# Kernel tuning notes

Measured on AMD Instinct MI355X. Metric: run time of the kernel, lower is better.

Reference implementation:

```python
import jax, jax.numpy as jnp
import numpy as np

NEG_INF = -1e9
LRELU_SLOPE = 0.2


def setup_inputs() -> dict:
    N, F_IN, F_OUT = 8192, 256, 128
    key = jax.random.key(0)
    k_adj, k_x, k_w, k_phi = jax.random.split(key, 4)
    adj = (jax.random.uniform(k_adj, (N, N)) < 0.01).astype(jnp.float32)
    x = jax.random.normal(k_x, (N, F_IN), dtype=jnp.float32)
    stdv_w = 1.0 / np.sqrt(F_OUT)
    weight = jax.random.uniform(k_w, (F_IN, F_OUT), minval=-stdv_w, maxval=stdv_w, dtype=jnp.float32)
    bias = jnp.zeros((F_OUT,), dtype=jnp.float32)
    phi = jax.random.uniform(k_phi, (2 * F_OUT, 1), minval=-1.0, maxval=1.0, dtype=jnp.float32)
    return {"adj": adj, "input": x, "weight": weight, "bias": bias, "phi": phi}


def reference(adj, input, weight, bias, phi):
    # x_prime: [N, F_OUT]
    x_prime = input @ weight + bias
    N = adj.shape[0]
    F_out = x_prime.shape[1]
    # S[i, j] = cat(x_i, x_j) @ phi = x_i @ phi[:F] + x_j @ phi[F:]
    # (identical math to the repeat+cat formulation, without the O(N^2*2F) tensor)
    phi_src = phi[:F_out, 0]  # [F_OUT]
    phi_dst = phi[F_out:, 0]  # [F_OUT]
    s_src = x_prime @ phi_src  # [N]
    s_dst = x_prime @ phi_dst  # [N]
    S = s_src[:, None] + s_dst[None, :]  # [N, N]
    S = jnp.where(S >= 0, S, LRELU_SLOPE * S)  # leaky_relu(0.2)
    mask = (adj + jnp.eye(N, dtype=adj.dtype)) > 0
    S_masked = jnp.where(mask, S, NEG_INF)
    attention = jax.nn.softmax(S_masked, axis=1)  # row-wise
    h = attention @ x_prime  # [N, F_OUT]
    return h
```

## Files before the change

kernel.cpp:

```cpp
#include <hip/hip_runtime.h>

#define Nn    8192
#define FIN   256
#define FOUTc 128
#define MAXN  512

typedef float f32x4 __attribute__((ext_vector_type(4)));

__global__ __launch_bounds__(256) void k_xp(const float* __restrict__ x,
                                            const float* __restrict__ w,
                                            const float* __restrict__ bias,
                                            const float* __restrict__ phi,
                                            float* __restrict__ xp,
                                            float* __restrict__ s_src,
                                            float* __restrict__ s_dst)
{
    const int wave = blockIdx.x * 4 + (threadIdx.x >> 6);
    const int lane = threadIdx.x & 63;
    const int row0 = wave * 8;

    const float2 bv = ((const float2*)bias)[lane];
    const float2 ps = ((const float2*)phi)[lane];
    const float2 pd = ((const float2*)(phi + FOUTc))[lane];

    const float* xr = x + (size_t)row0 * FIN;
    float2 acc[8];
#pragma unroll
    for (int r = 0; r < 8; r++) acc[r] = make_float2(0.f, 0.f);

#pragma unroll 4
    for (int k = 0; k < FIN; k++) {
        const float2 wv = ((const float2*)(w + (size_t)k * FOUTc))[lane];
#pragma unroll
        for (int r = 0; r < 8; r++) {
            const float xv = xr[r * FIN + k];
            acc[r].x = fmaf(xv, wv.x, acc[r].x);
            acc[r].y = fmaf(xv, wv.y, acc[r].y);
        }
    }

#pragma unroll
    for (int r = 0; r < 8; r++) {
        const float2 h = make_float2(acc[r].x + bv.x, acc[r].y + bv.y);
        ((float2*)(xp + (size_t)(row0 + r) * FOUTc))[lane] = h;
        float a = h.x * ps.x + h.y * ps.y;
        float b = h.x * pd.x + h.y * pd.y;
#pragma unroll
        for (int off = 32; off > 0; off >>= 1) {
            a += __shfl_down(a, off, 64);
            b += __shfl_down(b, off, 64);
        }
        if (lane == 0) { s_src[row0 + r] = a; s_dst[row0 + r] = b; }
    }
}

__global__ __launch_bounds__(256) void k_agg(const float* __restrict__ adj,
                                             const float* __restrict__ xp,
                                             const float* __restrict__ s_src,
                                             const float* __restrict__ s_dst,
                                             float* __restrict__ out)
{
    __shared__ int   nbr[MAXN];
    __shared__ float wts[MAXN];
    __shared__ float hp[2][FOUTc];
    __shared__ float sinv;
    __shared__ int   cnt;

    const int tid = threadIdx.x;
    const int i = blockIdx.x;
    if (tid == 0) cnt = 0;
    __syncthreads();

    const f32x4* arow4 = (const f32x4*)(adj + (size_t)i * Nn);
    f32x4 buf[8];
#pragma unroll
    for (int t = 0; t < 8; t++) buf[t] = __builtin_nontemporal_load(arow4 + t * 256 + tid);

#pragma unroll
    for (int t = 0; t < 8; t++) {
        const int j0 = (t * 256 + tid) * 4;
#pragma unroll
        for (int p = 0; p < 4; p++) {
            const int j = j0 + p;
            if (buf[t][p] != 0.f || j == i) {
                const int pos = atomicAdd(&cnt, 1);
                if (pos < MAXN) nbr[pos] = j;
            }
        }
    }
    __syncthreads();
    const int L    = (cnt < MAXN) ? cnt : MAXN;
    const int Lpad = (L + 7) & ~7;
    if (tid < Lpad - L) { nbr[L + tid] = i; wts[L + tid] = 0.f; }

    if (tid < 64) {
        const float ssi = s_src[i];
        float lmax = -1e30f;
        for (int n = tid; n < L; n += 64) {
            const float sd = s_dst[nbr[n]];
            wts[n] = sd;
            lmax = fmaxf(lmax, sd);
        }
#pragma unroll
        for (int off = 32; off > 0; off >>= 1)
            lmax = fmaxf(lmax, __shfl_xor(lmax, off, 64));
        const float Sm  = ssi + lmax;
        const float m_i = (Sm >= 0.f) ? Sm : 0.2f * Sm;
        float lsum = 0.f;
        for (int n = tid; n < L; n += 64) {
            float S = ssi + wts[n];
            S = (S >= 0.f) ? S : 0.2f * S;
            const float wv = __expf(S - m_i);
            wts[n] = wv;
            lsum += wv;
        }
#pragma unroll
        for (int off = 32; off > 0; off >>= 1) lsum += __shfl_xor(lsum, off, 64);
        if (tid == 0) sinv = 1.f / lsum;
    }
    __syncthreads();
    const float inv = sinv;

    const int o  = tid & 127;
    const int g  = tid >> 7;
    const int Lh = Lpad >> 1;
    const int base = g * Lh;
    const float* xpo = xp + o;
    float h0 = 0.f, h1 = 0.f, h2 = 0.f, h3 = 0.f;
    for (int n = base; n < base + Lh; n += 4) {
        const int   j0 = nbr[n],   j1 = nbr[n+1], j2 = nbr[n+2], j3 = nbr[n+3];
        const float w0 = wts[n],   w1 = wts[n+1], w2 = wts[n+2], w3 = wts[n+3];
        h0 = fmaf(w0, xpo[(size_t)j0 * FOUTc], h0);
        h1 = fmaf(w1, xpo[(size_t)j1 * FOUTc], h1);
        h2 = fmaf(w2, xpo[(size_t)j2 * FOUTc], h2);
        h3 = fmaf(w3, xpo[(size_t)j3 * FOUTc], h3);
    }
    hp[g][o] = (h0 + h1) + (h2 + h3);
    __syncthreads();
    if (tid < FOUTc)
        out[(size_t)i * FOUTc + tid] = (hp[0][tid] + hp[1][tid]) * inv;
}

extern "C" void kernel_launch(void* const* d_in, const int* in_sizes, int n_in,
                              void* d_out, int out_size, void* d_ws, size_t ws_size,
                              hipStream_t stream)
{
    (void)out_size; (void)ws_size;
    const float* adj  = (const float*)d_in[0];
    const float* x    = (const float*)d_in[1];
    const float* w    = (const float*)d_in[2];
    const float* bias = (const float*)d_in[3];
    const float* phi  = (const float*)d_in[4];
    for (int i = 0; i < n_in; i++) {
        switch (in_sizes[i]) {
            case Nn * Nn:     adj  = (const float*)d_in[i]; break;
            case Nn * FIN:    x    = (const float*)d_in[i]; break;
            case FIN * FOUTc: w    = (const float*)d_in[i]; break;
            case FOUTc:       bias = (const float*)d_in[i]; break;
            case 2 * FOUTc:   phi  = (const float*)d_in[i]; break;
        }
    }
    float* out = (float*)d_out;

    float* xp    = (float*)d_ws;
    float* s_src = xp + (size_t)Nn * FOUTc;
    float* s_dst = s_src + Nn;

    hipLaunchKernelGGL(k_xp,  dim3(256), dim3(256), 0, stream,
                       x, w, bias, phi, xp, s_src, s_dst);
    hipLaunchKernelGGL(k_agg, dim3(Nn),  dim3(256), 0, stream,
                       adj, xp, s_src, s_dst, out);
}
```

Baseline: 415.0 us.

## Warp-specialize aggregation: one wave compacts next adjacency row while others aggregate

The aggregation kernel now handles four rows per block with 192 threads. One wave scans and compacts the adjacency row for the next row into a double-buffered shared list, while two waves compute the softmax and the weighted gather for the current row. The goal is to overlap streaming the 256MB adjacency matrix with the gather and softmax work, and to cut per-block overhead. The tradeoff is that a single wave now streams each 32KB row, which may limit memory-level parallelism, and there are fewer blocks (2048) in flight.

Result: slower. 453.7 us (+9.3%).

```diff
diff --git a/kernel.cpp b/kernel.cpp
--- a/kernel.cpp
+++ b/kernel.cpp
@@ -4,6 +4,7 @@
 #define FIN   256
 #define FOUTc 128
 #define MAXN  512
+#define RPB   4
 
 typedef float f32x4 __attribute__((ext_vector_type(4)));
 
@@ -54,91 +55,123 @@
     }
 }
 
-__global__ __launch_bounds__(256) void k_agg(const float* __restrict__ adj,
+__device__ __forceinline__ void compact_row(const float* __restrict__ adj, int row,
+                                            int* __restrict__ nbrb, int* __restrict__ cnt,
+                                            int lane)
+{
+    const f32x4* arow4 = (const f32x4*)(adj + (size_t)row * Nn);
+#pragma unroll 1
+    for (int c = 0; c < 4; c++) {
+        f32x4 buf[8];
+#pragma unroll
+        for (int k = 0; k < 8; k++)
+            buf[k] = __builtin_nontemporal_load(arow4 + c * 512 + k * 64 + lane);
+#pragma unroll
+        for (int k = 0; k < 8; k++) {
+            const int j0 = (c * 512 + k * 64 + lane) * 4;
+#pragma unroll
+            for (int p = 0; p < 4; p++) {
+                const int j = j0 + p;
+                if (buf[k][p] != 0.f || j == row) {
+                    const int pos = atomicAdd(cnt, 1);
+                    if (pos < MAXN) nbrb[pos] = j;
+                }
+            }
+        }
+    }
+}
+
+__global__ __launch_bounds__(192) void k_agg(const float* __restrict__ adj,
                                              const float* __restrict__ xp,
                                              const float* __restrict__ s_src,
                                              const float* __restrict__ s_dst,
                                              float* __restrict__ out)
 {
-    __shared__ int   nbr[MAXN];
-    __shared__ float wts[MAXN];
-    __shared__ float hp[2][FOUTc];
-    __shared__ float sinv;
-    __shared__ int   cnt;
-
-    const int tid = threadIdx.x;
-    const int i = blockIdx.x;
-    if (tid == 0) cnt = 0;
+    __shared__ int   nbr[2][MAXN];
+    __shared__ float wts[2][MAXN];
+    __shared__ int   cnts[2];
+
+    const int tid  = threadIdx.x;
+    const int lane = tid & 63;
+    const int row0 = blockIdx.x * RPB;
+
+    if (tid == 0) { cnts[0] = 0; cnts[1] = 0; }
     __syncthreads();
 
-    const f32x4* arow4 = (const f32x4*)(adj + (size_t)i * Nn);
-    f32x4 buf[8];
-#pragma unroll
-    for (int t = 0; t < 8; t++) buf[t] = __builtin_nontemporal_load(arow4 + t * 256 + tid);
-
-#pragma unroll
-    for (int t = 0; t < 8; t++) {
-        const int j0 = (t * 256 + tid) * 4;
-#pragma unroll
-        for (int p = 0; p < 4; p++) {
-            const int j = j0 + p;
-            if (buf[t][p] != 0.f || j == i) {
-                const int pos = atomicAdd(&cnt, 1);
-                if (pos < MAXN) nbr[pos] = j;
-            }
-        }
-    }
+    if (tid >= 128) compact_row(adj, row0, nbr[0], &cnts[0], lane);
     __syncthreads();
-    const int L    = (cnt < MAXN) ? cnt : MAXN;
-    const int Lpad = (L + 7) & ~7;
-    if (tid < Lpad - L) { nbr[L + tid] = i; wts[L + tid] = 0.f; }
-
-    if (tid < 64) {
-        const float ssi = s_src[i];
-        float lmax = -1e30f;
-        for (int n = tid; n < L; n += 64) {
-            const float sd = s_dst[nbr[n]];
-            wts[n] = sd;
-            lmax = fmaxf(lmax, sd);
-        }
-#pragma unroll
-        for (int off = 32; off > 0; off >>= 1)
-            lmax = fmaxf(lmax, __shfl_xor(lmax, off, 64));
-        const float Sm  = ssi + lmax;
-        const float m_i = (Sm >= 0.f) ? Sm : 0.2f * Sm;
-        float lsum = 0.f;
-        for (int n = tid; n < L; n += 64) {
-            float S = ssi + wts[n];
-            S = (S >= 0.f) ? S : 0.2f * S;
-            const float wv = __expf(S - m_i);
-            wts[n] = wv;
-            lsum += wv;
-        }
-#pragma unroll
-        for (int off = 32; off > 0; off >>= 1) lsum += __shfl_xor(lsum, off, 64);
-        if (tid == 0) sinv = 1.f / lsum;
-    }
-    __syncthreads();
-    const float inv = sinv;
-
-    const int o  = tid & 127;
-    const int g  = tid >> 7;
-    const int Lh = Lpad >> 1;
-    const int base = g * Lh;
-    const float* xpo = xp + o;
-    float h0 = 0.f, h1 = 0.f, h2 = 0.f, h3 = 0.f;
-    for (int n = base; n < base + Lh; n += 4) {
-        const int   j0 = nbr[n],   j1 = nbr[n+1], j2 = nbr[n+2], j3 = nbr[n+3];
-        const float w0 = wts[n],   w1 = wts[n+1], w2 = wts[n+2], w3 = wts[n+3];
-        h0 = fmaf(w0, xpo[(size_t)j0 * FOUTc], h0);
-        h1 = fmaf(w1, xpo[(size_t)j1 * FOUTc], h1);
-        h2 = fmaf(w2, xpo[(size_t)j2 * FOUTc], h2);
-        h3 = fmaf(w3, xpo[(size_t)j3 * FOUTc], h3);
-    }
-    hp[g][o] = (h0 + h1) + (h2 + h3);
-    __syncthreads();
-    if (tid < FOUTc)
-        out[(size_t)i * FOUTc + tid] = (hp[0][tid] + hp[1][tid]) * inv;
+
+    for (int t = 0; t < RPB; t++) {
+        const int cur = t & 1;
+        const int row = row0 + t;
+
+        if (tid >= 128) {
+            if (t + 1 < RPB) {
+                const int nxt = cur ^ 1;
+                if (lane == 0) cnts[nxt] = 0;
+                compact_row(adj, row + 1, nbr[nxt], &cnts[nxt], lane);
+            }
+        } else {
+            const int Lr   = cnts[cur];
+            const int L    = (Lr < MAXN) ? Lr : MAXN;
+            const int Lpad = (L + 3) & ~3;
+            const float ssi = s_src[row];
+
+            float sdv[8];
+            float lmax = -1e30f;
+#pragma unroll
+            for (int q = 0; q < 8; q++) {
+                const int n = lane + 64 * q;
+                sdv[q] = -1e30f;
+                if (n < L) {
+                    sdv[q] = s_dst[nbr[cur][n]];
+                    lmax = fmaxf(lmax, sdv[q]);
+                }
+            }
+#pragma unroll
+            for (int off = 32; off > 0; off >>= 1)
+                lmax = fmaxf(lmax, __shfl_xor(lmax, off, 64));
+            const float Sm  = ssi + lmax;
+            const float m_i = (Sm >= 0.f) ? Sm : 0.2f * Sm;
+
+            float lsum = 0.f;
+#pragma unroll
+            for (int q = 0; q < 8; q++) {
+                const int n = lane + 64 * q;
+                if (n < L) {
+                    float S = ssi + sdv[q];
+                    S = (S >= 0.f) ? S : 0.2f * S;
+                    const float e = __expf(S - m_i);
+                    wts[cur][n] = e;
+                    lsum += e;
+                }
+            }
+#pragma unroll
+            for (int off = 32; off > 0; off >>= 1) lsum += __shfl_xor(lsum, off, 64);
+            const float inv = 1.f / lsum;
+
+            for (int n = L + lane; n < Lpad; n += 64) {
+                nbr[cur][n] = row;
+                wts[cur][n] = 0.f;
+            }
+
+            const int o = tid;
+            const float* xpo = xp + o;
+            float h0 = 0.f, h1 = 0.f, h2 = 0.f, h3 = 0.f;
+            for (int n = 0; n < Lpad; n += 4) {
+                const int   j0 = nbr[cur][n],     j1 = nbr[cur][n + 1];
+                const int   j2 = nbr[cur][n + 2], j3 = nbr[cur][n + 3];
+                const float w0 = wts[cur][n],     w1 = wts[cur][n + 1];
+                const float w2 = wts[cur][n + 2], w3 = wts[cur][n + 3];
+                h0 = fmaf(w0, xpo[(size_t)j0 * FOUTc], h0);
+                h1 = fmaf(w1, xpo[(size_t)j1 * FOUTc], h1);
+                h2 = fmaf(w2, xpo[(size_t)j2 * FOUTc], h2);
+                h3 = fmaf(w3, xpo[(size_t)j3 * FOUTc], h3);
+            }
+            out[(size_t)row * FOUTc + o] = ((h0 + h1) + (h2 + h3)) * inv;
+        }
+        __syncthreads();
+    }
 }
 
 extern "C" void kernel_launch(void* const* d_in, const int* in_sizes, int n_in,
@@ -166,8 +199,8 @@
     float* s_src = xp + (size_t)Nn * FOUTc;
     float* s_dst = s_src + Nn;
 
-    hipLaunchKernelGGL(k_xp,  dim3(256), dim3(256), 0, stream,
+    hipLaunchKernelGGL(k_xp,  dim3(256),    dim3(256), 0, stream,
                        x, w, bias, phi, xp, s_src, s_dst);
-    hipLaunchKernelGGL(k_agg, dim3(Nn),  dim3(256), 0, stream,
+    hipLaunchKernelGGL(k_agg, dim3(Nn/RPB), dim3(192), 0, stream,
                        adj, xp, s_src, s_dst, out);
 }
```

## Overlap adjacency compaction with feature projection and split aggregation into CSR pass

Applied to the files above, without the earlier changes.

The adjacency scan that builds per-row neighbor lists now runs inside the first kernel, alongside the x@W projection blocks. It writes a padded CSR-like list to workspace, so the dominant 256MB adjacency read can overlap with the GEMM instead of waiting for it. A second kernel reads the compact lists to do the softmax and aggregation, and the max/sum reductions now use all four waves instead of one. The cost is an extra round-trip of neighbor indices through global memory, an additional kernel, and more workspace use.

Result: no change. 412.9 us (-0.5%).

```diff
diff --git a/kernel.cpp b/kernel.cpp
--- a/kernel.cpp
+++ b/kernel.cpp
@@ -1,73 +1,71 @@
 #include <hip/hip_runtime.h>
 
-#define Nn    8192
-#define FIN   256
-#define FOUTc 128
-#define MAXN  512
+#define Nn     8192
+#define FIN    256
+#define FOUTc  128
+#define MAXN   512
+#define LCAP   504
+#define NXPB   256
 
 typedef float f32x4 __attribute__((ext_vector_type(4)));
 
-__global__ __launch_bounds__(256) void k_xp(const float* __restrict__ x,
-                                            const float* __restrict__ w,
-                                            const float* __restrict__ bias,
-                                            const float* __restrict__ phi,
-                                            float* __restrict__ xp,
-                                            float* __restrict__ s_src,
-                                            float* __restrict__ s_dst)
+__global__ __launch_bounds__(256) void k1(const float* __restrict__ adj,
+                                          const float* __restrict__ x,
+                                          const float* __restrict__ w,
+                                          const float* __restrict__ bias,
+                                          const float* __restrict__ phi,
+                                          float* __restrict__ xp,
+                                          float* __restrict__ s_src,
+                                          float* __restrict__ s_dst,
+                                          int* __restrict__ csr,
+                                          int* __restrict__ csr_cnt)
 {
-    const int wave = blockIdx.x * 4 + (threadIdx.x >> 6);
-    const int lane = threadIdx.x & 63;
-    const int row0 = wave * 8;
-
-    const float2 bv = ((const float2*)bias)[lane];
-    const float2 ps = ((const float2*)phi)[lane];
-    const float2 pd = ((const float2*)(phi + FOUTc))[lane];
-
-    const float* xr = x + (size_t)row0 * FIN;
-    float2 acc[8];
-#pragma unroll
-    for (int r = 0; r < 8; r++) acc[r] = make_float2(0.f, 0.f);
+    __shared__ int nbr[MAXN];
+    __shared__ int cnt;
+    const int tid = threadIdx.x;
+    const int bid = blockIdx.x;
+
+    if (bid < NXPB) {
+        const int wave = bid * 4 + (tid >> 6);
+        const int lane = tid & 63;
+        const int row0 = wave * 8;
+
+        const float2 bv = ((const float2*)bias)[lane];
+        const float2 ps = ((const float2*)phi)[lane];
+        const float2 pd = ((const float2*)(phi + FOUTc))[lane];
+
+        const float* xr = x + (size_t)row0 * FIN;
+        float2 acc[8];
+#pragma unroll
+        for (int r = 0; r < 8; r++) acc[r] = make_float2(0.f, 0.f);
 
 #pragma unroll 4
-    for (int k = 0; k < FIN; k++) {
-        const float2 wv = ((const float2*)(w + (size_t)k * FOUTc))[lane];
+        for (int k = 0; k < FIN; k++) {
+            const float2 wv = ((const float2*)(w + (size_t)k * FOUTc))[lane];
+#pragma unroll
+            for (int r = 0; r < 8; r++) {
+                const float xv = xr[r * FIN + k];
+                acc[r].x = fmaf(xv, wv.x, acc[r].x);
+                acc[r].y = fmaf(xv, wv.y, acc[r].y);
+            }
+        }
 #pragma unroll
         for (int r = 0; r < 8; r++) {
-            const float xv = xr[r * FIN + k];
-            acc[r].x = fmaf(xv, wv.x, acc[r].x);
-            acc[r].y = fmaf(xv, wv.y, acc[r].y);
-        }
-    }
-
-#pragma unroll
-    for (int r = 0; r < 8; r++) {
-        const float2 h = make_float2(acc[r].x + bv.x, acc[r].y + bv.y);
-        ((float2*)(xp + (size_t)(row0 + r) * FOUTc))[lane] = h;
-        float a = h.x * ps.x + h.y * ps.y;
-        float b = h.x * pd.x + h.y * pd.y;
-#pragma unroll
-        for (int off = 32; off > 0; off >>= 1) {
-            a += __shfl_down(a, off, 64);
-            b += __shfl_down(b, off, 64);
-        }
-        if (lane == 0) { s_src[row0 + r] = a; s_dst[row0 + r] = b; }
-    }
-}
-
-__global__ __launch_bounds__(256) void k_agg(const float* __restrict__ adj,
-                                             const float* __restrict__ xp,
-                                             const float* __restrict__ s_src,
-                                             const float* __restrict__ s_dst,
-                                             float* __restrict__ out)
-{
-    __shared__ int   nbr[MAXN];
-    __shared__ float wts[MAXN];
-    __shared__ float hp[2][FOUTc];
-    __shared__ float sinv;
-    __shared__ int   cnt;
-
-    const int tid = threadIdx.x;
-    const int i = blockIdx.x;
+            const float2 h = make_float2(acc[r].x + bv.x, acc[r].y + bv.y);
+            ((float2*)(xp + (size_t)(row0 + r) * FOUTc))[lane] = h;
+            float a = h.x * ps.x + h.y * ps.y;
+            float b = h.x * pd.x + h.y * pd.y;
+#pragma unroll
+            for (int off = 32; off > 0; off >>= 1) {
+                a += __shfl_down(a, off, 64);
+                b += __shfl_down(b, off, 64);
+            }
+            if (lane == 0) { s_src[row0 + r] = a; s_dst[row0 + r] = b; }
+        }
+        return;
+    }
+
+    const int i = bid - NXPB;
     if (tid == 0) cnt = 0;
     __syncthreads();
 
@@ -84,42 +82,76 @@
             const int j = j0 + p;
             if (buf[t][p] != 0.f || j == i) {
                 const int pos = atomicAdd(&cnt, 1);
-                if (pos < MAXN) nbr[pos] = j;
+                if (pos < LCAP) nbr[pos] = j;
             }
         }
     }
     __syncthreads();
-    const int L    = (cnt < MAXN) ? cnt : MAXN;
+    const int L    = (cnt < LCAP) ? cnt : LCAP;
     const int Lpad = (L + 7) & ~7;
-    if (tid < Lpad - L) { nbr[L + tid] = i; wts[L + tid] = 0.f; }
-
-    if (tid < 64) {
-        const float ssi = s_src[i];
-        float lmax = -1e30f;
-        for (int n = tid; n < L; n += 64) {
-            const float sd = s_dst[nbr[n]];
+    if (tid < Lpad - L) nbr[L + tid] = i;
+    __syncthreads();
+
+    int* crow = csr + (size_t)i * MAXN;
+    for (int n = tid; n < Lpad; n += 256) crow[n] = nbr[n];
+    if (tid == 0) csr_cnt[i] = L;
+}
+
+__global__ __launch_bounds__(256) void k2(const int* __restrict__ csr,
+                                          const int* __restrict__ csr_cnt,
+                                          const float* __restrict__ xp,
+                                          const float* __restrict__ s_src,
+                                          const float* __restrict__ s_dst,
+                                          float* __restrict__ out)
+{
+    __shared__ int   nbrs[MAXN];
+    __shared__ float wts[MAXN];
+    __shared__ float hp[2][FOUTc];
+    __shared__ float red_m[4];
+    __shared__ float red_s[4];
+
+    const int tid = threadIdx.x;
+    const int i = blockIdx.x;
+    const int L = csr_cnt[i];
+    const int Lpad = (L + 7) & ~7;
+    const int* crow = csr + (size_t)i * MAXN;
+    const float ssi = s_src[i];
+
+    float lmax = -1e30f;
+    for (int n = tid; n < Lpad; n += 256) {
+        const int j = crow[n];
+        nbrs[n] = j;
+        if (n < L) {
+            const float sd = s_dst[j];
             wts[n] = sd;
             lmax = fmaxf(lmax, sd);
-        }
-#pragma unroll
-        for (int off = 32; off > 0; off >>= 1)
-            lmax = fmaxf(lmax, __shfl_xor(lmax, off, 64));
-        const float Sm  = ssi + lmax;
-        const float m_i = (Sm >= 0.f) ? Sm : 0.2f * Sm;
-        float lsum = 0.f;
-        for (int n = tid; n < L; n += 64) {
-            float S = ssi + wts[n];
-            S = (S >= 0.f) ? S : 0.2f * S;
-            const float wv = __expf(S - m_i);
-            wts[n] = wv;
-            lsum += wv;
-        }
-#pragma unroll
-        for (int off = 32; off > 0; off >>= 1) lsum += __shfl_xor(lsum, off, 64);
-        if (tid == 0) sinv = 1.f / lsum;
-    }
-    __syncthreads();
-    const float inv = sinv;
+        } else {
+            wts[n] = 0.f;
+        }
+    }
+#pragma unroll
+    for (int off = 32; off > 0; off >>= 1)
+        lmax = fmaxf(lmax, __shfl_xor(lmax, off, 64));
+    if ((tid & 63) == 0) red_m[tid >> 6] = lmax;
+    __syncthreads();
+    const float maxd = fmaxf(fmaxf(red_m[0], red_m[1]), fmaxf(red_m[2], red_m[3]));
+    const float Sm   = ssi + maxd;
+    const float m_i  = (Sm >= 0.f) ? Sm : 0.2f * Sm;
+
+    float lsum = 0.f;
+    for (int n = tid; n < L; n += 256) {
+        float S = ssi + wts[n];
+        S = (S >= 0.f) ? S : 0.2f * S;
+        const float e = __expf(S - m_i);
+        wts[n] = e;
+        lsum += e;
+    }
+#pragma unroll
+    for (int off = 32; off > 0; off >>= 1) lsum += __shfl_xor(lsum, off, 64);
+    if ((tid & 63) == 0) red_s[tid >> 6] = lsum;
+    __syncthreads();
+    const float l_i = (red_s[0] + red_s[1]) + (red_s[2] + red_s[3]);
+    const float inv = 1.f / l_i;
 
     const int o  = tid & 127;
     const int g  = tid >> 7;
@@ -128,8 +160,8 @@
     const float* xpo = xp + o;
     float h0 = 0.f, h1 = 0.f, h2 = 0.f, h3 = 0.f;
     for (int n = base; n < base + Lh; n += 4) {
-        const int   j0 = nbr[n],   j1 = nbr[n+1], j2 = nbr[n+2], j3 = nbr[n+3];
-        const float w0 = wts[n],   w1 = wts[n+1], w2 = wts[n+2], w3 = wts[n+3];
+        const int   j0 = nbrs[n],   j1 = nbrs[n+1], j2 = nbrs[n+2], j3 = nbrs[n+3];
+        const float w0 = wts[n],    w1 = wts[n+1],  w2 = wts[n+2],  w3 = wts[n+3];
         h0 = fmaf(w0, xpo[(size_t)j0 * FOUTc], h0);
         h1 = fmaf(w1, xpo[(size_t)j1 * FOUTc], h1);
         h2 = fmaf(w2, xpo[(size_t)j2 * FOUTc], h2);
@@ -162,12 +194,14 @@
     }
     float* out = (float*)d_out;
 
-    float* xp    = (float*)d_ws;
-    float* s_src = xp + (size_t)Nn * FOUTc;
-    float* s_dst = s_src + Nn;
-
-    hipLaunchKernelGGL(k_xp,  dim3(256), dim3(256), 0, stream,
-                       x, w, bias, phi, xp, s_src, s_dst);
-    hipLaunchKernelGGL(k_agg, dim3(Nn),  dim3(256), 0, stream,
-                       adj, xp, s_src, s_dst, out);
+    float* xp      = (float*)d_ws;
+    float* s_src   = xp + (size_t)Nn * FOUTc;
+    float* s_dst   = s_src + Nn;
+    int*   csr_cnt = (int*)(s_dst + Nn);
+    int*   csr     = csr_cnt + Nn;
+
+    hipLaunchKernelGGL(k1, dim3(NXPB + Nn), dim3(256), 0, stream,
+                       adj, x, w, bias, phi, xp, s_src, s_dst, csr, csr_cnt);
+    hipLaunchKernelGGL(k2, dim3(Nn),        dim3(256), 0, stream,
+                       csr, csr_cnt, xp, s_src, s_dst, out);
 }
```
